# Kernel optimization log

Hardware: AMD Instinct MI355X
Metric: run time of the kernel (lower is better)

The kernel has to match this reference:

```python
import jax, jax.numpy as jnp
import numpy as np

B, S, D = 2, 2048, 1024
H, KH = 16, 4            # query heads, kv heads
DK = D // H              # 64
REP = H // KH            # queries per kv head


def _rope(x):
    # x: (B, h, S, dk); non-interleaved rotate-half RoPE as in source
    dk = x.shape[-1]
    half = dk // 2
    seq = x.shape[2]
    theta = 10000.0 ** (-(jnp.arange(half, dtype=jnp.float32) / half))
    pos = jnp.arange(seq, dtype=jnp.float32)
    freqs = pos[:, None] * theta[None, :]          # (S, half)
    cos = jnp.cos(freqs)[None, None]               # (1,1,S,half)
    sin = jnp.sin(freqs)[None, None]
    x1, x2 = x[..., :half], x[..., half:]
    return jnp.concatenate([x1 * cos - x2 * sin, x2 * cos + x1 * sin], axis=-1)


def setup_inputs() -> dict:
    key = jax.random.key(0)
    ks = jax.random.split(key, 9)
    sd = 1.0 / np.sqrt(D)
    x = jax.random.normal(ks[0], (B, S, D), dtype=jnp.float32)
    # causal mask: 1 where attend allowed, 0 where masked (mask==0 -> -inf)
    mask = jnp.tril(jnp.ones((S, S), dtype=jnp.int32))[None, None]
    Wq = jax.random.normal(ks[1], (D, H * DK), dtype=jnp.float32) * sd
    bq = jnp.zeros((H * DK,), dtype=jnp.float32)
    Wk = jax.random.normal(ks[2], (D, KH * DK), dtype=jnp.float32) * sd
    bk = jnp.zeros((KH * DK,), dtype=jnp.float32)
    Wv = jax.random.normal(ks[3], (D, KH * DK), dtype=jnp.float32) * sd
    bv = jnp.zeros((KH * DK,), dtype=jnp.float32)
    Wo = jax.random.normal(ks[4], (H * DK, D), dtype=jnp.float32) * sd
    bo = jnp.zeros((D,), dtype=jnp.float32)
    return {"x": x, "mask": mask, "Wq": Wq, "bq": bq, "Wk": Wk, "bk": bk,
            "Wv": Wv, "bv": bv, "Wo": Wo, "bo": bo}


def reference(x, mask, Wq, bq, Wk, bk, Wv, bv, Wo, bo):
    b, s, _ = x.shape
    q = (x @ Wq + bq).reshape(b, s, H, DK).transpose(0, 2, 1, 3)   # (B,H,S,DK)
    k = (x @ Wk + bk).reshape(b, s, KH, DK).transpose(0, 2, 1, 3)  # (B,KH,S,DK)
    v = (x @ Wv + bv).reshape(b, s, KH, DK).transpose(0, 2, 1, 3)
    q = _rope(q)
    k = _rope(k)
    k = jnp.repeat(k, REP, axis=1)  # GQA expand: (B,H,S,DK)
    v = jnp.repeat(v, REP, axis=1)
    attn = jnp.einsum('bhqd,bhkd->bhqk', q, k) / np.sqrt(DK).astype(np.float32)
    attn = jnp.where(mask == 0, -jnp.inf, attn)
    score = jax.nn.softmax(attn, axis=-1)
    out = jnp.einsum('bhqk,bhkd->bhqd', score, v)   # (B,H,S,DK)
    out = out.transpose(0, 2, 1, 3).reshape(b, s, H * DK)
    return out @ Wo + bo
```

## Files before the change

kernel.cpp:

```cpp
#include <hip/hip_runtime.h>
#include <math.h>

#define B_   2
#define S_   2048
#define D_   1024
#define H_   16
#define KH_  4
#define DK_  64

using bf16x8 = __attribute__((ext_vector_type(8))) short;
using bf16x4 = __attribute__((ext_vector_type(4))) short;
using f32x4  = __attribute__((ext_vector_type(4))) float;
using u32x4  = __attribute__((ext_vector_type(4))) unsigned int;
using u32x2  = __attribute__((ext_vector_type(2))) unsigned int;

__device__ inline unsigned short f2bf(float f) {
    unsigned u = __float_as_uint(f);
    u += 0x7FFFu + ((u >> 16) & 1u);
    return (unsigned short)(u >> 16);
}
__device__ inline float bf2f(unsigned short u) {
    return __uint_as_float(((unsigned)u) << 16);
}

#ifdef __has_builtin
#if __has_builtin(__builtin_amdgcn_cvt_pk_bf16_f32)
#define PKBF16 1
#endif
#if __has_builtin(__builtin_amdgcn_exp2f)
#define NEXP2 1
#endif
#endif
__device__ inline unsigned pk2bf(float a, float b) {
#ifdef PKBF16
    auto r = __builtin_amdgcn_cvt_pk_bf16_f32(a, b);
    unsigned u; __builtin_memcpy(&u, &r, 4);
    return u;
#else
    return (unsigned)f2bf(a) | ((unsigned)f2bf(b) << 16);
#endif
}
__device__ inline float fexp2(float x) {
#ifdef NEXP2
    return __builtin_amdgcn_exp2f(x);
#else
    return exp2f(x);
#endif
}

#define GL16(gp, lp) __builtin_amdgcn_global_load_lds( \
    (const __attribute__((address_space(1))) unsigned int*)(gp), \
    (__attribute__((address_space(3))) unsigned int*)(lp), 16, 0, 0)

__global__ __launch_bounds__(256) void prep_kernel(
    const float* __restrict__ x,
    const float* __restrict__ Wq, const float* __restrict__ Wk,
    const float* __restrict__ Wv, const float* __restrict__ Wo,
    unsigned short* __restrict__ xb,
    unsigned short* __restrict__ WqkvT,
    unsigned short* __restrict__ WoT)
{
    __shared__ float T[64][65];
    const int t = threadIdx.x;
    int bx = blockIdx.x;

    if (bx < 2048) {
        const int i = bx * 256 + t;
        f32x4 a = *(const f32x4*)(x + (long)i * 8);
        f32x4 b = *(const f32x4*)(x + (long)i * 8 + 4);
        bf16x8 o;
        o[0] = (short)f2bf(a[0]); o[1] = (short)f2bf(a[1]);
        o[2] = (short)f2bf(a[2]); o[3] = (short)f2bf(a[3]);
        o[4] = (short)f2bf(b[0]); o[5] = (short)f2bf(b[1]);
        o[6] = (short)f2bf(b[2]); o[7] = (short)f2bf(b[3]);
        *(bf16x8*)(xb + (long)i * 8) = o;
        return;
    }
    bx -= 2048;
    const float* in; unsigned short* out; int C;
    if (bx < 256)      { in = Wq; out = WqkvT;               C = 1024; }
    else if (bx < 320) { in = Wk; out = WqkvT + 1024 * 1024; C = 256;  bx -= 256; }
    else if (bx < 384) { in = Wv; out = WqkvT + 1280 * 1024; C = 256;  bx -= 320; }
    else               { in = Wo; out = WoT;                 C = 1024; bx -= 384; }
    const int R  = 1024, nr = 16;
    const int r0 = (bx % nr) * 64;
    const int c0 = (bx / nr) * 64;
    {
        const int r  = t >> 2;
        const int cq = (t & 3) * 16;
        const float* src = in + (long)(r0 + r) * C + c0 + cq;
        #pragma unroll
        for (int i = 0; i < 4; ++i) {
            f32x4 v = *(const f32x4*)(src + i * 4);
            T[r][cq + i * 4 + 0] = v[0];
            T[r][cq + i * 4 + 1] = v[1];
            T[r][cq + i * 4 + 2] = v[2];
            T[r][cq + i * 4 + 3] = v[3];
        }
    }
    __syncthreads();
    {
        const int c  = t >> 2;
        const int rq = (t & 3) * 16;
        bf16x8 p0, p1;
        #pragma unroll
        for (int i = 0; i < 8; ++i) {
            p0[i] = (short)f2bf(T[rq + i][c]);
            p1[i] = (short)f2bf(T[rq + 8 + i][c]);
        }
        unsigned short* dst = out + (long)(c0 + c) * R + r0 + rq;
        *(bf16x8*)dst       = p0;
        *(bf16x8*)(dst + 8) = p1;
    }
}

template<bool BF16OUT>
__global__ __launch_bounds__(256) void gemm64_kernel(
    const unsigned short* __restrict__ A,
    const unsigned short* __restrict__ Bt,
    const float* __restrict__ b0,
    const float* __restrict__ b1,
    const float* __restrict__ b2,
    float* __restrict__ outf,
    unsigned short* __restrict__ outb,
    int N, int K)
{
    __shared__ unsigned short As[2][64][64];
    __shared__ unsigned short Bs[2][128][64];

    const int t  = threadIdx.x;
    const int m0 = blockIdx.x * 64;
    const int n0 = blockIdx.y * 128;

    const int w    = t >> 6;
    const int lane = t & 63;
    const int n    = lane & 15;
    const int quad = lane >> 4;
    const int wm   = (w >> 1) * 32;
    const int wn   = (w & 1) * 64;

    const int sr8 = lane >> 3;
    const int gch = (lane & 7) ^ sr8;

    const unsigned short* gA = A  + (long)(m0 + w * 8 + sr8) * K + gch * 8;
    const unsigned short* gB = Bt + (long)(n0 + w * 8 + sr8) * K + gch * 8;

    #define STAGE(buf, kk)                                              \
    do {                                                                \
        GL16(gA + (kk),              &As[buf][w * 8][0]);               \
        GL16(gA + 32 * K + (kk),     &As[buf][w * 8 + 32][0]);          \
        GL16(gB + (kk),              &Bs[buf][w * 8][0]);               \
        GL16(gB + 32 * K + (kk),     &Bs[buf][w * 8 + 32][0]);          \
        GL16(gB + 64 * K + (kk),     &Bs[buf][w * 8 + 64][0]);          \
        GL16(gB + 96 * K + (kk),     &Bs[buf][w * 8 + 96][0]);          \
    } while (0)

    STAGE(0, 0);

    f32x4 acc[2][4];
    #pragma unroll
    for (int i = 0; i < 2; ++i)
        #pragma unroll
        for (int j = 0; j < 4; ++j) acc[i][j] = 0.0f;

    const int n7 = n & 7;

    for (int k0 = 0; k0 < K; k0 += 64) {
        const int cur = (k0 >> 6) & 1;
        __syncthreads();
        if (k0 + 64 < K) STAGE(cur ^ 1, k0 + 64);

        #pragma unroll
        for (int kp = 0; kp < 2; ++kp) {
            const int ca = ((kp * 4 + quad) ^ n7) * 8;
            bf16x8 af[2], bfr[4];
            #pragma unroll
            for (int i = 0; i < 2; ++i)
                af[i] = *(const bf16x8*)&As[cur][wm + i * 16 + n][ca];
            #pragma unroll
            for (int j = 0; j < 4; ++j)
                bfr[j] = *(const bf16x8*)&Bs[cur][wn + j * 16 + n][ca];
            #pragma unroll
            for (int mi = 0; mi < 2; ++mi)
                #pragma unroll
                for (int ni = 0; ni < 4; ++ni)
                    acc[mi][ni] = __builtin_amdgcn_mfma_f32_16x16x32_bf16(
                        af[mi], bfr[ni], acc[mi][ni], 0, 0, 0);
        }
    }
    #undef STAGE

    #pragma unroll
    for (int mi = 0; mi < 2; ++mi) {
        #pragma unroll
        for (int r = 0; r < 4; ++r) {
            const int gm = m0 + wm + mi * 16 + quad * 4 + r;
            #pragma unroll
            for (int ni = 0; ni < 4; ++ni) {
                const int gn = n0 + wn + ni * 16 + n;
                if (BF16OUT) {
                    const float b = (gn < 1024) ? b0[gn]
                                  : (gn < 1280) ? b1[gn - 1024]
                                                : b2[gn - 1280];
                    outb[(long)gm * N + gn] = f2bf(acc[mi][ni][r] + b);
                } else {
                    outf[(long)gm * N + gn] = acc[mi][ni][r] + b0[gn];
                }
            }
        }
    }
}

__global__ __launch_bounds__(256) void scatter_kernel(
    const unsigned short* __restrict__ qkvm,
    unsigned short* __restrict__ qbuf,
    unsigned short* __restrict__ kbuf,
    unsigned short* __restrict__ vbuf)
{
    __shared__ unsigned short T[64][72];
    const int t = threadIdx.x;
    int bx = blockIdx.x;

    if (bx < 1280) {
        const int idx = bx * 256 + t;
        const int m   = idx / 80;
        const int rem = idx - m * 80;
        const int h20 = rem >> 2;
        const int d0  = (rem & 3) * 8;

        const int s  = m & (S_ - 1);
        const int bb = m >> 11;
        const int col0 = (h20 < 16) ? h20 * 64 + d0 : 1024 + (h20 - 16) * 64 + d0;
        const float scl = (h20 < 16) ? 0.1803368801111606f : 1.0f;

        const bf16x8 x1v = *(const bf16x8*)(qkvm + (long)m * 1536 + col0);
        const bf16x8 x2v = *(const bf16x8*)(qkvm + (long)m * 1536 + col0 + 32);
        bf16x8 o1, o2;
        #pragma unroll
        for (int j = 0; j < 8; ++j) {
            const int d = d0 + j;
            const float theta = exp2f(-(float)d * (13.287712379549449f / 32.0f));
            const float f = (float)s * theta;
            const float c = cosf(f) * scl, sn = sinf(f) * scl;
            const float x1 = bf2f((unsigned short)x1v[j]);
            const float x2 = bf2f((unsigned short)x2v[j]);
            o1[j] = (short)f2bf(x1 * c - x2 * sn);
            o2[j] = (short)f2bf(x2 * c + x1 * sn);
        }
        unsigned short* dst = (h20 < 16)
            ? qbuf + ((long)(bb * H_ + h20) * S_ + s) * DK_ + d0
            : kbuf + ((long)(bb * KH_ + (h20 - 16)) * S_ + s) * DK_ + d0;
        *(bf16x8*)dst        = o1;
        *(bf16x8*)(dst + 32) = o2;
        return;
    }
    bx -= 1280;
    const int bkh = bx >> 5;
    const int s0  = (bx & 31) * 64;
    {
        const int s  = t >> 2;
        const int dq = (t & 3) * 16;
        const unsigned short* src =
            qkvm + (long)((bkh >> 2) * S_ + s0 + s) * 1536 + 1280 + (bkh & 3) * 64 + dq;
        *(bf16x8*)&T[s][dq]     = *(const bf16x8*)src;
        *(bf16x8*)&T[s][dq + 8] = *(const bf16x8*)(src + 8);
    }
    __syncthreads();
    {
        const int d  = t >> 2;
        const int sq = (t & 3) * 16;
        bf16x8 p0, p1;
        #pragma unroll
        for (int i = 0; i < 8; ++i) {
            p0[i] = (short)T[sq + i][d];
            p1[i] = (short)T[sq + 8 + i][d];
        }
        unsigned short* dst = vbuf + ((long)bkh * DK_ + d) * S_ + s0 + sq;
        *(bf16x8*)dst       = p0;
        *(bf16x8*)(dst + 8) = p1;
    }
}

__global__ __launch_bounds__(256) void attn_kernel(
    const unsigned short* __restrict__ qb,
    const unsigned short* __restrict__ kbf,
    const unsigned short* __restrict__ vT,
    unsigned short* __restrict__ ot)
{
    __shared__ __align__(16) unsigned short Ks[2][64][64];
    __shared__ __align__(16) unsigned short Vs[2][64][64];
    __shared__ __align__(16) unsigned short Ps[4][16][64];

    const int tid = threadIdx.x;
    const int bx  = blockIdx.x;

    const int j  = bx >> 8;
    const int p  = bx & 255;
    const int g  = p >> 5;
    const int bh = p & 31;
    int qt;
    if      (j == 0) qt = 31 - g;
    else if (j == 1) qt = 16 + g;
    else if (j == 2) qt = 15 - g;
    else             qt = g;

    const int b   = bh >> 4, h = bh & 15;
    const int kh  = h >> 2;
    const int q0  = qt * 64;

    const int wv   = tid >> 6;
    const int lane = tid & 63;
    const int n    = lane & 15;
    const int quad = lane >> 4;
    const int xk   = n & 7;

    const unsigned short* qp =
        qb + ((long)(b * H_ + h) * S_ + q0 + wv * 16 + n) * DK_;
    const bf16x8 qa0 = *(const bf16x8*)(qp + quad * 8);
    const bf16x8 qa1 = *(const bf16x8*)(qp + 32 + quad * 8);

    f32x4 O[4];
    #pragma unroll
    for (int dt = 0; dt < 4; ++dt) O[dt] = 0.0f;
    float lsum = 0.f;

    const unsigned short* kbase = kbf + (long)(b * KH_ + kh) * S_ * DK_;
    const unsigned short* vbase = vT  + (long)(b * KH_ + kh) * DK_ * S_;

    const int ntiles = qt + 1;
    const int srow = tid >> 3;
    const int lc   = tid & 7;
    const int sc8  = lc * 8;
    const int pcs  = (lc ^ (srow & 7)) * 8;

    u32x4 kr0 = *(const u32x4*)(kbase + (long)srow * DK_ + sc8);
    u32x4 kr1 = *(const u32x4*)(kbase + (long)(32 + srow) * DK_ + sc8);
    u32x4 vr0 = *(const u32x4*)(vbase + (long)srow * S_ + sc8);
    u32x4 vr1 = *(const u32x4*)(vbase + (long)(32 + srow) * S_ + sc8);
    *(u32x4*)&Ks[0][srow][pcs]      = kr0;
    *(u32x4*)&Ks[0][32 + srow][pcs] = kr1;
    *(u32x4*)&Vs[0][srow][pcs]      = vr0;
    *(u32x4*)&Vs[0][32 + srow][pcs] = vr1;

    for (int u = 0; u < ntiles; ++u) {
        const int cur = u & 1;
        const int kb  = u * 64;
        __syncthreads();

        if (u + 1 < ntiles) {
            const int kbn = kb + 64;
            kr0 = *(const u32x4*)(kbase + (long)(kbn + srow) * DK_ + sc8);
            kr1 = *(const u32x4*)(kbase + (long)(kbn + 32 + srow) * DK_ + sc8);
            vr0 = *(const u32x4*)(vbase + (long)srow * S_ + kbn + sc8);
            vr1 = *(const u32x4*)(vbase + (long)(32 + srow) * S_ + kbn + sc8);
        }

        f32x4 sc[4];
        #pragma unroll
        for (int ct = 0; ct < 4; ++ct) {
            const bf16x8 kf0 =
                *(const bf16x8*)&Ks[cur][ct * 16 + n][(quad ^ xk) * 8];
            const bf16x8 kf1 =
                *(const bf16x8*)&Ks[cur][ct * 16 + n][((quad + 4) ^ xk) * 8];
            f32x4 c = 0.0f;
            c = __builtin_amdgcn_mfma_f32_16x16x32_bf16(kf0, qa0, c, 0, 0, 0);
            c = __builtin_amdgcn_mfma_f32_16x16x32_bf16(kf1, qa1, c, 0, 0, 0);
            sc[ct] = c;
        }

        if (u == qt) {
            const int qg = q0 + wv * 16 + n;
            #pragma unroll
            for (int ct = 0; ct < 4; ++ct) {
                const int kq = kb + ct * 16 + quad * 4;
                #pragma unroll
                for (int r = 0; r < 4; ++r)
                    if (kq + r > qg) sc[ct][r] = -INFINITY;
            }
        }
        f32x4 rs4 = 0.0f;
        #pragma unroll
        for (int ct = 0; ct < 4; ++ct) {
            #pragma unroll
            for (int r = 0; r < 4; ++r) {
                const float p2 = fexp2(sc[ct][r]);
                sc[ct][r] = p2;
                rs4[r] += p2;
            }
        }
        lsum += (rs4[0] + rs4[1]) + (rs4[2] + rs4[3]);

        #pragma unroll
        for (int ct = 0; ct < 4; ++ct) {
            u32x2 pw;
            pw[0] = pk2bf(sc[ct][0], sc[ct][1]);
            pw[1] = pk2bf(sc[ct][2], sc[ct][3]);
            const int pc = ((2 * ct + (quad >> 1)) ^ xk) * 8 + (quad & 1) * 4;
            *(u32x2*)&Ps[wv][n][pc] = pw;
        }
        const bf16x8 pb0 = *(const bf16x8*)&Ps[wv][n][(quad ^ xk) * 8];
        const bf16x8 pb1 = *(const bf16x8*)&Ps[wv][n][((quad + 4) ^ xk) * 8];

        #pragma unroll
        for (int dt = 0; dt < 4; ++dt) {
            const bf16x8 av0 =
                *(const bf16x8*)&Vs[cur][dt * 16 + n][(quad ^ xk) * 8];
            const bf16x8 av1 =
                *(const bf16x8*)&Vs[cur][dt * 16 + n][((quad + 4) ^ xk) * 8];
            O[dt] = __builtin_amdgcn_mfma_f32_16x16x32_bf16(av0, pb0, O[dt], 0, 0, 0);
            O[dt] = __builtin_amdgcn_mfma_f32_16x16x32_bf16(av1, pb1, O[dt], 0, 0, 0);
        }

        if (u + 1 < ntiles) {
            const int nb = cur ^ 1;
            *(u32x4*)&Ks[nb][srow][pcs]      = kr0;
            *(u32x4*)&Ks[nb][32 + srow][pcs] = kr1;
            *(u32x4*)&Vs[nb][srow][pcs]      = vr0;
            *(u32x4*)&Vs[nb][32 + srow][pcs] = vr1;
        }
    }

    lsum += __shfl_xor(lsum, 16);
    lsum += __shfl_xor(lsum, 32);
    const float inv = 1.0f / lsum;
    #pragma unroll
    for (int dt = 0; dt < 4; ++dt) {
        u32x2 pw;
        pw[0] = pk2bf(O[dt][0] * inv, O[dt][1] * inv);
        pw[1] = pk2bf(O[dt][2] * inv, O[dt][3] * inv);
        const int pc = ((2 * dt + (quad >> 1)) ^ xk) * 8 + (quad & 1) * 4;
        *(u32x2*)&Ps[wv][n][pc] = pw;
    }
    const int fr = lane >> 3;
    const int c8l = lane & 7;
    #pragma unroll
    for (int it = 0; it < 2; ++it) {
        const int row = it * 8 + fr;
        const int q   = q0 + wv * 16 + row;
        unsigned short* op = ot + ((long)(b * S_ + q) * H_ + h) * DK_ + c8l * 8;
        *(bf16x8*)op = *(const bf16x8*)&Ps[wv][row][(c8l ^ fr) * 8];
    }
}

extern "C" void kernel_launch(void* const* d_in, const int* in_sizes, int n_in,
                              void* d_out, int out_size, void* d_ws, size_t ws_size,
                              hipStream_t stream)
{
    const float* x  = (const float*)d_in[0];
    const float* Wq = (const float*)d_in[2];
    const float* bq = (const float*)d_in[3];
    const float* Wk = (const float*)d_in[4];
    const float* bk = (const float*)d_in[5];
    const float* Wv = (const float*)d_in[6];
    const float* bv = (const float*)d_in[7];
    const float* Wo = (const float*)d_in[8];
    const float* bo = (const float*)d_in[9];
    float* out = (float*)d_out;

    unsigned short* ws    = (unsigned short*)d_ws;
    unsigned short* xb    = ws;
    unsigned short* qkvm  = xb + 4194304;
    unsigned short* qbuf  = qkvm + 6291456;
    unsigned short* kbuf  = qbuf + 4194304;
    unsigned short* vbuf  = kbuf + 1048576;
    unsigned short* WqkvT = vbuf + 1048576;
    unsigned short* WoT   = WqkvT + 1572864;
    unsigned short* ob    = qkvm;

    prep_kernel<<<2688, 256, 0, stream>>>(x, Wq, Wk, Wv, Wo, xb, WqkvT, WoT);

    gemm64_kernel<true><<<dim3(64, 12), 256, 0, stream>>>(
        xb, WqkvT, bq, bk, bv, nullptr, qkvm, 1536, 1024);

    scatter_kernel<<<1536, 256, 0, stream>>>(qkvm, qbuf, kbuf, vbuf);

    attn_kernel<<<B_ * H_ * (S_ / 64), 256, 0, stream>>>(qbuf, kbuf, vbuf, ob);

    gemm64_kernel<false><<<dim3(64, 8), 256, 0, stream>>>(
        ob, WoT, bo, nullptr, nullptr, out, nullptr, 1024, 1024);
}
```

Before: 178.9 us.

## Process 128 query rows per attention block with eight waves sharing K/V tiles

The attention kernel now uses 512-thread blocks of eight waves, each block covering 128 query rows instead of 64. Every K/V tile staged in LDS is shared by twice as many query rows, which halves global K/V loads and staging work per query. The grid shrinks to 512 blocks, and the per-block causal ordering is simplified to a pairing of mirrored 128-row tiles. The lower four waves sit idle through the final diagonal tile, and fewer, larger blocks may reduce scheduling flexibility.

```diff
diff --git a/kernel.cpp b/kernel.cpp
--- a/kernel.cpp
+++ b/kernel.cpp
@@ -281,7 +281,7 @@
     }
 }
 
-__global__ __launch_bounds__(256) void attn_kernel(
+__global__ __launch_bounds__(512) void attn_kernel(
     const unsigned short* __restrict__ qb,
     const unsigned short* __restrict__ kbf,
     const unsigned short* __restrict__ vT,
@@ -289,7 +289,7 @@
 {
     __shared__ __align__(16) unsigned short Ks[2][64][64];
     __shared__ __align__(16) unsigned short Vs[2][64][64];
-    __shared__ __align__(16) unsigned short Ps[4][16][64];
+    __shared__ __align__(16) unsigned short Ps[8][16][64];
 
     const int tid = threadIdx.x;
     const int bx  = blockIdx.x;
@@ -298,15 +298,11 @@
     const int p  = bx & 255;
     const int g  = p >> 5;
     const int bh = p & 31;
-    int qt;
-    if      (j == 0) qt = 31 - g;
-    else if (j == 1) qt = 16 + g;
-    else if (j == 2) qt = 15 - g;
-    else             qt = g;
+    const int a  = j ? g : (15 - g);
 
     const int b   = bh >> 4, h = bh & 15;
     const int kh  = h >> 2;
-    const int q0  = qt * 64;
+    const int q0  = a * 128;
 
     const int wv   = tid >> 6;
     const int lane = tid & 63;
@@ -327,20 +323,17 @@
     const unsigned short* kbase = kbf + (long)(b * KH_ + kh) * S_ * DK_;
     const unsigned short* vbase = vT  + (long)(b * KH_ + kh) * DK_ * S_;
 
-    const int ntiles = qt + 1;
+    const int ntiles = 2 * a + 2;
+    const int ub     = 2 * a + (wv >> 2);
     const int srow = tid >> 3;
     const int lc   = tid & 7;
     const int sc8  = lc * 8;
     const int pcs  = (lc ^ (srow & 7)) * 8;
 
-    u32x4 kr0 = *(const u32x4*)(kbase + (long)srow * DK_ + sc8);
-    u32x4 kr1 = *(const u32x4*)(kbase + (long)(32 + srow) * DK_ + sc8);
-    u32x4 vr0 = *(const u32x4*)(vbase + (long)srow * S_ + sc8);
-    u32x4 vr1 = *(const u32x4*)(vbase + (long)(32 + srow) * S_ + sc8);
-    *(u32x4*)&Ks[0][srow][pcs]      = kr0;
-    *(u32x4*)&Ks[0][32 + srow][pcs] = kr1;
-    *(u32x4*)&Vs[0][srow][pcs]      = vr0;
-    *(u32x4*)&Vs[0][32 + srow][pcs] = vr1;
+    u32x4 kr = *(const u32x4*)(kbase + (long)srow * DK_ + sc8);
+    u32x4 vr = *(const u32x4*)(vbase + (long)srow * S_ + sc8);
+    *(u32x4*)&Ks[0][srow][pcs] = kr;
+    *(u32x4*)&Vs[0][srow][pcs] = vr;
 
     for (int u = 0; u < ntiles; ++u) {
         const int cur = u & 1;
@@ -349,74 +342,73 @@
 
         if (u + 1 < ntiles) {
             const int kbn = kb + 64;
-            kr0 = *(const u32x4*)(kbase + (long)(kbn + srow) * DK_ + sc8);
-            kr1 = *(const u32x4*)(kbase + (long)(kbn + 32 + srow) * DK_ + sc8);
-            vr0 = *(const u32x4*)(vbase + (long)srow * S_ + kbn + sc8);
-            vr1 = *(const u32x4*)(vbase + (long)(32 + srow) * S_ + kbn + sc8);
-        }
-
-        f32x4 sc[4];
-        #pragma unroll
-        for (int ct = 0; ct < 4; ++ct) {
-            const bf16x8 kf0 =
-                *(const bf16x8*)&Ks[cur][ct * 16 + n][(quad ^ xk) * 8];
-            const bf16x8 kf1 =
-                *(const bf16x8*)&Ks[cur][ct * 16 + n][((quad + 4) ^ xk) * 8];
-            f32x4 c = 0.0f;
-            c = __builtin_amdgcn_mfma_f32_16x16x32_bf16(kf0, qa0, c, 0, 0, 0);
-            c = __builtin_amdgcn_mfma_f32_16x16x32_bf16(kf1, qa1, c, 0, 0, 0);
-            sc[ct] = c;
-        }
-
-        if (u == qt) {
-            const int qg = q0 + wv * 16 + n;
+            kr = *(const u32x4*)(kbase + (long)(kbn + srow) * DK_ + sc8);
+            vr = *(const u32x4*)(vbase + (long)srow * S_ + kbn + sc8);
+        }
+
+        if (u <= ub) {
+            f32x4 sc[4];
             #pragma unroll
             for (int ct = 0; ct < 4; ++ct) {
-                const int kq = kb + ct * 16 + quad * 4;
+                const bf16x8 kf0 =
+                    *(const bf16x8*)&Ks[cur][ct * 16 + n][(quad ^ xk) * 8];
+                const bf16x8 kf1 =
+                    *(const bf16x8*)&Ks[cur][ct * 16 + n][((quad + 4) ^ xk) * 8];
+                f32x4 c = 0.0f;
+                c = __builtin_amdgcn_mfma_f32_16x16x32_bf16(kf0, qa0, c, 0, 0, 0);
+                c = __builtin_amdgcn_mfma_f32_16x16x32_bf16(kf1, qa1, c, 0, 0, 0);
+                sc[ct] = c;
+            }
+
+            if (u == ub) {
+                const int qg = q0 + wv * 16 + n;
                 #pragma unroll
-                for (int r = 0; r < 4; ++r)
-                    if (kq + r > qg) sc[ct][r] = -INFINITY;
-            }
-        }
-        f32x4 rs4 = 0.0f;
-        #pragma unroll
-        for (int ct = 0; ct < 4; ++ct) {
-            #pragma unroll
-            for (int r = 0; r < 4; ++r) {
-                const float p2 = fexp2(sc[ct][r]);
-                sc[ct][r] = p2;
-                rs4[r] += p2;
-            }
-        }
-        lsum += (rs4[0] + rs4[1]) + (rs4[2] + rs4[3]);
-
-        #pragma unroll
-        for (int ct = 0; ct < 4; ++ct) {
-            u32x2 pw;
-            pw[0] = pk2bf(sc[ct][0], sc[ct][1]);
-            pw[1] = pk2bf(sc[ct][2], sc[ct][3]);
-            const int pc = ((2 * ct + (quad >> 1)) ^ xk) * 8 + (quad & 1) * 4;
-            *(u32x2*)&Ps[wv][n][pc] = pw;
-        }
-        const bf16x8 pb0 = *(const bf16x8*)&Ps[wv][n][(quad ^ xk) * 8];
-        const bf16x8 pb1 = *(const bf16x8*)&Ps[wv][n][((quad + 4) ^ xk) * 8];
-
-        #pragma unroll
-        for (int dt = 0; dt < 4; ++dt) {
-            const bf16x8 av0 =
-                *(const bf16x8*)&Vs[cur][dt * 16 + n][(quad ^ xk) * 8];
-            const bf16x8 av1 =
-                *(const bf16x8*)&Vs[cur][dt * 16 + n][((quad + 4) ^ xk) * 8];
-            O[dt] = __builtin_amdgcn_mfma_f32_16x16x32_bf16(av0, pb0, O[dt], 0, 0, 0);
-            O[dt] = __builtin_amdgcn_mfma_f32_16x16x32_bf16(av1, pb1, O[dt], 0, 0, 0);
+                for (int ct = 0; ct < 4; ++ct) {
+                    const int kq = kb + ct * 16 + quad * 4;
+                    #pragma unroll
+                    for (int r = 0; r < 4; ++r)
+                        if (kq + r > qg) sc[ct][r] = -INFINITY;
+                }
+            }
+
+            f32x4 rs4 = 0.0f;
+            #pragma unroll
+            for (int ct = 0; ct < 4; ++ct) {
+                #pragma unroll
+                for (int r = 0; r < 4; ++r) {
+                    const float p2 = fexp2(sc[ct][r]);
+                    sc[ct][r] = p2;
+                    rs4[r] += p2;
+                }
+            }
+            lsum += (rs4[0] + rs4[1]) + (rs4[2] + rs4[3]);
+
+            #pragma unroll
+            for (int ct = 0; ct < 4; ++ct) {
+                u32x2 pw;
+                pw[0] = pk2bf(sc[ct][0], sc[ct][1]);
+                pw[1] = pk2bf(sc[ct][2], sc[ct][3]);
+                const int pc = ((2 * ct + (quad >> 1)) ^ xk) * 8 + (quad & 1) * 4;
+                *(u32x2*)&Ps[wv][n][pc] = pw;
+            }
+            const bf16x8 pb0 = *(const bf16x8*)&Ps[wv][n][(quad ^ xk) * 8];
+            const bf16x8 pb1 = *(const bf16x8*)&Ps[wv][n][((quad + 4) ^ xk) * 8];
+
+            #pragma unroll
+            for (int dt = 0; dt < 4; ++dt) {
+                const bf16x8 av0 =
+                    *(const bf16x8*)&Vs[cur][dt * 16 + n][(quad ^ xk) * 8];
+                const bf16x8 av1 =
+                    *(const bf16x8*)&Vs[cur][dt * 16 + n][((quad + 4) ^ xk) * 8];
+                O[dt] = __builtin_amdgcn_mfma_f32_16x16x32_bf16(av0, pb0, O[dt], 0, 0, 0);
+                O[dt] = __builtin_amdgcn_mfma_f32_16x16x32_bf16(av1, pb1, O[dt], 0, 0, 0);
+            }
         }
 
         if (u + 1 < ntiles) {
             const int nb = cur ^ 1;
-            *(u32x4*)&Ks[nb][srow][pcs]      = kr0;
-            *(u32x4*)&Ks[nb][32 + srow][pcs] = kr1;
-            *(u32x4*)&Vs[nb][srow][pcs]      = vr0;
-            *(u32x4*)&Vs[nb][32 + srow][pcs] = vr1;
+            *(u32x4*)&Ks[nb][srow][pcs] = kr;
+            *(u32x4*)&Vs[nb][srow][pcs] = vr;
         }
     }
 
@@ -431,6 +423,7 @@
         const int pc = ((2 * dt + (quad >> 1)) ^ xk) * 8 + (quad & 1) * 4;
         *(u32x2*)&Ps[wv][n][pc] = pw;
     }
+    __builtin_amdgcn_s_waitcnt(0);
     const int fr = lane >> 3;
     const int c8l = lane & 7;
     #pragma unroll
@@ -474,7 +467,7 @@
 
     scatter_kernel<<<1536, 256, 0, stream>>>(qkvm, qbuf, kbuf, vbuf);
 
-    attn_kernel<<<B_ * H_ * (S_ / 64), 256, 0, stream>>>(qbuf, kbuf, vbuf, ob);
+    attn_kernel<<<512, 512, 0, stream>>>(qbuf, kbuf, vbuf, ob);
 
     gemm64_kernel<false><<<dim3(64, 8), 256, 0, stream>>>(
         ob, WoT, bo, nullptr, nullptr, out, nullptr, 1024, 1024);
```

Result: no change. 177.2 us (-0.9%).
